# Performance work log

Hardware: AMD Instinct MI355X
Metric: run time of the kernel (lower is better)

The kernel has to match this reference:

```python
import jax, jax.numpy as jnp
import numpy as np

B, S, F, H, W = 16, 2048, 512, 512, 5
PAD = W // 2


def setup_inputs() -> dict:
    key = jax.random.key(0)
    k = jax.random.split(key, 6)
    scale = 0.02
    return {
        "embeds_output": jax.random.normal(k[0], (B, S, F), dtype=jnp.float32),
        "Wq": jax.random.normal(k[1], (F, H), dtype=jnp.float32) * scale,
        "Wk": jax.random.normal(k[2], (F, H), dtype=jnp.float32) * scale,
        "v_att": jax.random.normal(k[3], (H,), dtype=jnp.float32) * scale,
        "cnn_W": jax.random.normal(k[4], (W * F, H), dtype=jnp.float32) * scale,
        "cnn_b": jax.random.normal(k[5], (H,), dtype=jnp.float32) * scale,
    }


def reference(embeds_output, Wq, Wk, v_att, cnn_W, cnn_b):
    b, s, f = embeds_output.shape
    # getConvEmbeds: zero-pad and gather W shifted views -> [B, S, W, F]
    xp = jnp.pad(embeds_output, ((0, 0), (PAD, PAD), (0, 0)))
    windows = jnp.stack([xp[:, i:i + s, :] for i in range(W)], axis=2)  # [B,S,W,F]
    entity = windows[:, :, PAD, :]  # center token, [B,S,F]
    # Bahdanau additive attention over the window
    q = jnp.einsum('bsf,fh->bsh', entity, Wq)          # [B,S,H]
    kproj = jnp.einsum('bswf,fh->bswh', windows, Wk)   # [B,S,W,H]
    scores = jnp.einsum('bswh,h->bsw', jnp.tanh(kproj + q[:, :, None, :]), v_att)
    att = jax.nn.softmax(scores, axis=-1)              # [B,S,W]
    # weight contexts, flatten window dim (row-major W*F, matching torch reshape)
    att_context = (att[..., None] * windows).reshape(b, s, W * F)
    return att_context @ cnn_W + cnn_b                 # [B,S,H]
```

## Files before the change

### kernel.cpp

```cpp
#include <hip/hip_runtime.h>
#include <stdint.h>
#include <stddef.h>

typedef unsigned short u16;
typedef __attribute__((ext_vector_type(8))) short s16x8;
typedef __attribute__((ext_vector_type(8))) unsigned short u16x8;
typedef __attribute__((ext_vector_type(4))) unsigned short u16x4;
typedef __attribute__((ext_vector_type(4))) float f32x4;

typedef __attribute__((address_space(3))) void* as3_void_p;
typedef const __attribute__((address_space(1))) void* as1_cvoid_p;

#define GLD16(gp, lp) __builtin_amdgcn_global_load_lds((as1_cvoid_p)(gp), (as3_void_p)(lp), 16, 0, 0)

enum {
  NS = 2048, NF = 512, NH = 512, NW = 5,
  NROW = 32768,
  K2 = NW * NF
};

__device__ __forceinline__ u16 f2bf(float f) {
  unsigned u = __float_as_uint(f);
  u += 0x7FFFu + ((u >> 16) & 1u);
  return (u16)(u >> 16);
}
__device__ __forceinline__ float bf2f(u16 v) {
  return __uint_as_float(((unsigned)v) << 16);
}


__global__ __launch_bounds__(256) void cvtX(const float* __restrict__ X, u16* __restrict__ Xb) {
  int i = blockIdx.x * 256 + threadIdx.x;
  f32x4 v = ((const f32x4*)X)[i];
  u16x4 o;
  o.x = f2bf(v.x); o.y = f2bf(v.y); o.z = f2bf(v.z); o.w = f2bf(v.w);
  ((u16x4*)Xb)[i] = o;
}

__global__ __launch_bounds__(256) void cvtW(const float* __restrict__ Wq, const float* __restrict__ Wk,
                                            const float* __restrict__ cnnW,
                                            u16* __restrict__ Wt1, u16* __restrict__ Wt2) {
  int i = blockIdx.x * 256 + threadIdx.x;
  if (i < 1024 * 512) {
    int j = i >> 9, f = i & 511;
    float v = (j < 512) ? Wq[(size_t)f * 512 + j] : Wk[(size_t)f * 512 + (j - 512)];
    Wt1[i] = f2bf(v);
  } else {
    int t = i - 1024 * 512;
    int h = t / K2, k = t % K2;
    Wt2[t] = f2bf(cnnW[(size_t)k * 512 + h]);
  }
}


__global__ __launch_bounds__(512, 4) void gemm_qk(const u16* __restrict__ Xb,
                                                  const u16* __restrict__ Wt1,
                                                  u16* __restrict__ QKb) {
  __shared__ u16 As[2][128 * 64];
  __shared__ u16 Bs[2][128 * 64];
  const int tid  = threadIdx.x;
  const int lane = tid & 63, wid = tid >> 6;
  const int wr = wid >> 2, wc = wid & 3;
  const int fr = lane & 15, fq = lane >> 4;
  const int wgid = (blockIdx.x & 7) * 256 + (blockIdx.x >> 3);
  const int brow = (wgid >> 3) * 128;
  const int bcol = (wgid & 7) * 128;

  const int rsub = tid >> 3;
  const int cb   = (((tid & 7) ^ (rsub & 7)) << 4);
  const char* gA0 = (const char*)(Xb  + (size_t)(brow + rsub) * NF) + cb;
  const char* gA1 = (const char*)(Xb  + (size_t)(brow + 64 + rsub) * NF) + cb;
  const char* gB0 = (const char*)(Wt1 + (size_t)(bcol + rsub) * NF) + cb;
  const char* gB1 = (const char*)(Wt1 + (size_t)(bcol + 64 + rsub) * NF) + cb;

  f32x4 acc[4][2] = {};

  GLD16(gA0, (char*)As[0] + tid * 16);
  GLD16(gA1, (char*)As[0] + 8192 + tid * 16);
  GLD16(gB0, (char*)Bs[0] + tid * 16);
  GLD16(gB1, (char*)Bs[0] + 8192 + tid * 16);
  __syncthreads();

  int cur = 0;
  for (int kt = 0; kt < 8; ++kt) {
    if (kt + 1 < 8) {
      int o = (kt + 1) * 128;
      GLD16(gA0 + o, (char*)As[cur ^ 1] + tid * 16);
      GLD16(gA1 + o, (char*)As[cur ^ 1] + 8192 + tid * 16);
      GLD16(gB0 + o, (char*)Bs[cur ^ 1] + tid * 16);
      GLD16(gB1 + o, (char*)Bs[cur ^ 1] + 8192 + tid * 16);
    }
    const char* Ab = (const char*)As[cur];
    const char* Bb = (const char*)Bs[cur];
#pragma unroll
    for (int kk = 0; kk < 2; ++kk) {
      s16x8 af[4], bfr[2];
#pragma unroll
      for (int m = 0; m < 4; ++m) {
        int row = wr * 64 + m * 16 + fr;
        af[m] = *(const s16x8*)(Ab + row * 128 + ((kk * 64 + fq * 16) ^ ((row & 7) << 4)));
      }
#pragma unroll
      for (int n = 0; n < 2; ++n) {
        int row = wc * 32 + n * 16 + fr;
        bfr[n] = *(const s16x8*)(Bb + row * 128 + ((kk * 64 + fq * 16) ^ ((row & 7) << 4)));
      }
#pragma unroll
      for (int m = 0; m < 4; ++m)
#pragma unroll
        for (int n = 0; n < 2; ++n)
          acc[m][n] = __builtin_amdgcn_mfma_f32_16x16x32_bf16(af[m], bfr[n], acc[m][n], 0, 0, 0);
    }
    __syncthreads();
    cur ^= 1;
  }

#pragma unroll
  for (int m = 0; m < 4; ++m)
#pragma unroll
    for (int n = 0; n < 2; ++n)
#pragma unroll
      for (int r = 0; r < 4; ++r) {
        int row = brow + wr * 64 + m * 16 + fq * 4 + r;
        int col = bcol + wc * 32 + n * 16 + fr;
        QKb[(size_t)row * 1024 + col] = f2bf(acc[m][n][r]);
      }
}


__global__ __launch_bounds__(256) void scores_att(const u16* __restrict__ QKb,
                                                  const float* __restrict__ vatt,
                                                  float* __restrict__ att) {
  const int lane = threadIdx.x & 63;
  const int wid  = threadIdx.x >> 6;
  const int n = blockIdx.x * 4 + wid;
  const int s = n & (NS - 1);
  const int h0 = lane * 8;

  u16x8 qv = *(const u16x8*)(QKb + (size_t)n * 1024 + h0);
  f32x4 va0 = *(const f32x4*)(vatt + h0);
  f32x4 va1 = *(const f32x4*)(vatt + h0 + 4);
  float q[8], vv[8];
#pragma unroll
  for (int j = 0; j < 8; ++j) q[j] = bf2f(qv[j]);
  vv[0] = va0.x; vv[1] = va0.y; vv[2] = va0.z; vv[3] = va0.w;
  vv[4] = va1.x; vv[5] = va1.y; vv[6] = va1.z; vv[7] = va1.w;

  float sc[5];
#pragma unroll
  for (int w = 0; w < 5; ++w) {
    int sp = s + w - 2;
    u16x8 kv = {0, 0, 0, 0, 0, 0, 0, 0};
    if (sp >= 0 && sp < NS)
      kv = *(const u16x8*)(QKb + (size_t)(n + w - 2) * 1024 + 512 + h0);
    float acc = 0.f;
#pragma unroll
    for (int j = 0; j < 8; ++j) {
      float x = q[j] + bf2f(kv[j]);
      x = fminf(fmaxf(x, -15.f), 15.f);
      float e = __expf(2.f * x);
      acc += vv[j] * ((e - 1.f) / (e + 1.f));
    }
    sc[w] = acc;
  }
#pragma unroll
  for (int w = 0; w < 5; ++w)
#pragma unroll
    for (int o = 32; o > 0; o >>= 1)
      sc[w] += __shfl_xor(sc[w], o, 64);

  if (lane == 0) {
    float m = sc[0];
#pragma unroll
    for (int w = 1; w < 5; ++w) m = fmaxf(m, sc[w]);
    float e[5], sum = 0.f;
#pragma unroll
    for (int w = 0; w < 5; ++w) { e[w] = __expf(sc[w] - m); sum += e[w]; }
    float inv = 1.f / sum;
#pragma unroll
    for (int w = 0; w < 5; ++w) att[(size_t)n * 5 + w] = e[w] * inv;
  }
}


__global__ __launch_bounds__(512, 4) void gemm_out(const u16* __restrict__ Xb,
                                                   const u16* __restrict__ Wt2,
                                                   const float* __restrict__ att,
                                                   const float* __restrict__ cnnb,
                                                   float* __restrict__ out) {
  __shared__ u16 As[2][128 * 64];
  __shared__ u16 Bs[2][128 * 64];
  __shared__ float att_s[128 * 5];
  const int tid  = threadIdx.x;
  const int lane = tid & 63, wid = tid >> 6;
  const int wr = wid >> 2, wc = wid & 3;
  const int fr = lane & 15, fq = lane >> 4;
  const int wgid = (blockIdx.x & 7) * 128 + (blockIdx.x >> 3);
  const int brow = (wgid >> 2) * 128;
  const int bcol = (wgid & 3) * 128;

  if (tid < 128) {
    int s = (brow + tid) & (NS - 1);
#pragma unroll
    for (int w = 0; w < 5; ++w) {
      int sp = s + w - 2;
      att_s[tid * 5 + w] = (sp >= 0 && sp < NS) ? att[(size_t)(brow + tid) * 5 + w] : 0.f;
    }
  }

  const int rsub = tid >> 3;
  const int cb   = (((tid & 7) ^ (rsub & 7)) << 4);
  const char* gB0 = (const char*)(Wt2 + (size_t)(bcol + rsub) * K2) + cb;
  const char* gB1 = (const char*)(Wt2 + (size_t)(bcol + 64 + rsub) * K2) + cb;

  auto stage = [&](int buf, int it) {
    int wn = it >> 3, ktn = it & 7;
    int g0 = brow + rsub + wn - 2;
    int g1 = brow + 64 + rsub + wn - 2;
    g0 = g0 < 0 ? 0 : (g0 >= NROW ? NROW - 1 : g0);
    g1 = g1 < 0 ? 0 : (g1 >= NROW ? NROW - 1 : g1);
    int ko = ktn * 128;
    GLD16((const char*)(Xb + (size_t)g0 * NF) + cb + ko, (char*)As[buf] + tid * 16);
    GLD16((const char*)(Xb + (size_t)g1 * NF) + cb + ko, (char*)As[buf] + 8192 + tid * 16);
    GLD16(gB0 + wn * 1024 + ko, (char*)Bs[buf] + tid * 16);
    GLD16(gB1 + wn * 1024 + ko, (char*)Bs[buf] + 8192 + tid * 16);
  };

  f32x4 acc[4][2] = {};
  f32x4 accOut[4][2] = {};

  stage(0, 0);
  __syncthreads();

  int cur = 0;
  for (int it = 0; it < 40; ++it) {
    if (it + 1 < 40) stage(cur ^ 1, it + 1);
    const char* Ab = (const char*)As[cur];
    const char* Bb = (const char*)Bs[cur];
#pragma unroll
    for (int kk = 0; kk < 2; ++kk) {
      s16x8 af[4], bfr[2];
#pragma unroll
      for (int m = 0; m < 4; ++m) {
        int row = wr * 64 + m * 16 + fr;
        af[m] = *(const s16x8*)(Ab + row * 128 + ((kk * 64 + fq * 16) ^ ((row & 7) << 4)));
      }
#pragma unroll
      for (int n = 0; n < 2; ++n) {
        int row = wc * 32 + n * 16 + fr;
        bfr[n] = *(const s16x8*)(Bb + row * 128 + ((kk * 64 + fq * 16) ^ ((row & 7) << 4)));
      }
#pragma unroll
      for (int m = 0; m < 4; ++m)
#pragma unroll
        for (int n = 0; n < 2; ++n)
          acc[m][n] = __builtin_amdgcn_mfma_f32_16x16x32_bf16(af[m], bfr[n], acc[m][n], 0, 0, 0);
    }
    if ((it & 7) == 7) {
      int w = it >> 3;
#pragma unroll
      for (int m = 0; m < 4; ++m) {
        float a0 = att_s[(wr * 64 + m * 16 + fq * 4 + 0) * 5 + w];
        float a1 = att_s[(wr * 64 + m * 16 + fq * 4 + 1) * 5 + w];
        float a2 = att_s[(wr * 64 + m * 16 + fq * 4 + 2) * 5 + w];
        float a3 = att_s[(wr * 64 + m * 16 + fq * 4 + 3) * 5 + w];
#pragma unroll
        for (int n = 0; n < 2; ++n) {
          accOut[m][n][0] += a0 * acc[m][n][0];
          accOut[m][n][1] += a1 * acc[m][n][1];
          accOut[m][n][2] += a2 * acc[m][n][2];
          accOut[m][n][3] += a3 * acc[m][n][3];
          acc[m][n] = f32x4{0.f, 0.f, 0.f, 0.f};
        }
      }
    }
    __syncthreads();
    cur ^= 1;
  }

#pragma unroll
  for (int m = 0; m < 4; ++m)
#pragma unroll
    for (int n = 0; n < 2; ++n)
#pragma unroll
      for (int r = 0; r < 4; ++r) {
        int row = brow + wr * 64 + m * 16 + fq * 4 + r;
        int col = bcol + wc * 32 + n * 16 + fr;
        out[(size_t)row * NH + col] = accOut[m][n][r] + cnnb[col];
      }
}


extern "C" void kernel_launch(void* const* d_in, const int* in_sizes, int n_in,
                              void* d_out, int out_size, void* d_ws, size_t ws_size,
                              hipStream_t stream) {
  const float* X    = (const float*)d_in[0];
  const float* Wq   = (const float*)d_in[1];
  const float* Wk   = (const float*)d_in[2];
  const float* vatt = (const float*)d_in[3];
  const float* cnnW = (const float*)d_in[4];
  const float* cnnb = (const float*)d_in[5];
  float* out = (float*)d_out;

  char* ws = (char*)d_ws;
  u16*   Xb  = (u16*)ws;
  u16*   Wt1 = (u16*)(ws + 33554432);
  u16*   Wt2 = (u16*)(ws + 34603008);
  u16*   QKb = (u16*)(ws + 37224448);
  float* att = (float*)(ws + 104333312);

  cvtX<<<dim3(NROW * NF / 4 / 256), dim3(256), 0, stream>>>(X, Xb);
  cvtW<<<dim3((1024 * 512 + 512 * K2) / 256), dim3(256), 0, stream>>>(Wq, Wk, cnnW, Wt1, Wt2);
  gemm_qk<<<dim3(2048), dim3(512), 0, stream>>>(Xb, Wt1, QKb);
  scores_att<<<dim3(NROW / 4), dim3(256), 0, stream>>>(QKb, vatt, att);
  gemm_out<<<dim3(1024), dim3(512), 0, stream>>>(Xb, Wt2, att, cnnb, out);
}
```

Measured before the change: 215.2 us.

## Replace double-buffered BK=64 staging with single-buffered BK=128 tiles in both GEMMs

Both GEMM kernels drop the two-stage LDS double buffer with K-tiles of 64 and use a single buffer holding K-tiles of 128, loaded as four 32-row chunks per operand. This halves the number of K iterations and barriers per tile, while the LDS footprint stays the same. The cost is that global-to-LDS loads no longer overlap with MFMA work inside a block, so latency hiding now depends on other resident blocks. The output GEMM also restructures its loop into explicit window and K-tile nests.

```diff
diff --git a/kernel.cpp b/kernel.cpp
--- a/kernel.cpp
+++ b/kernel.cpp
@@ -56,8 +56,8 @@
 __global__ __launch_bounds__(512, 4) void gemm_qk(const u16* __restrict__ Xb,
                                                   const u16* __restrict__ Wt1,
                                                   u16* __restrict__ QKb) {
-  __shared__ u16 As[2][128 * 64];
-  __shared__ u16 Bs[2][128 * 64];
+  __shared__ u16 As[128 * 128];
+  __shared__ u16 Bs[128 * 128];
   const int tid  = threadIdx.x;
   const int lane = tid & 63, wid = tid >> 6;
   const int wr = wid >> 2, wc = wid & 3;
@@ -66,44 +66,38 @@
   const int brow = (wgid >> 3) * 128;
   const int bcol = (wgid & 7) * 128;
 
-  const int rsub = tid >> 3;
-  const int cb   = (((tid & 7) ^ (rsub & 7)) << 4);
-  const char* gA0 = (const char*)(Xb  + (size_t)(brow + rsub) * NF) + cb;
-  const char* gA1 = (const char*)(Xb  + (size_t)(brow + 64 + rsub) * NF) + cb;
-  const char* gB0 = (const char*)(Wt1 + (size_t)(bcol + rsub) * NF) + cb;
-  const char* gB1 = (const char*)(Wt1 + (size_t)(bcol + 64 + rsub) * NF) + cb;
+  const int rsub = tid >> 4;
+  const int scb  = ((tid & 15) << 4) ^ ((rsub & 7) << 4);
+  const char* gA[4];
+  const char* gB[4];
+#pragma unroll
+  for (int c = 0; c < 4; ++c) {
+    gA[c] = (const char*)(Xb  + (size_t)(brow + c * 32 + rsub) * NF) + scb;
+    gB[c] = (const char*)(Wt1 + (size_t)(bcol + c * 32 + rsub) * NF) + scb;
+  }
 
   f32x4 acc[4][2] = {};
 
-  GLD16(gA0, (char*)As[0] + tid * 16);
-  GLD16(gA1, (char*)As[0] + 8192 + tid * 16);
-  GLD16(gB0, (char*)Bs[0] + tid * 16);
-  GLD16(gB1, (char*)Bs[0] + 8192 + tid * 16);
-  __syncthreads();
-
-  int cur = 0;
-  for (int kt = 0; kt < 8; ++kt) {
-    if (kt + 1 < 8) {
-      int o = (kt + 1) * 128;
-      GLD16(gA0 + o, (char*)As[cur ^ 1] + tid * 16);
-      GLD16(gA1 + o, (char*)As[cur ^ 1] + 8192 + tid * 16);
-      GLD16(gB0 + o, (char*)Bs[cur ^ 1] + tid * 16);
-      GLD16(gB1 + o, (char*)Bs[cur ^ 1] + 8192 + tid * 16);
-    }
-    const char* Ab = (const char*)As[cur];
-    const char* Bb = (const char*)Bs[cur];
-#pragma unroll
-    for (int kk = 0; kk < 2; ++kk) {
+  for (int kt = 0; kt < 4; ++kt) {
+    const int ko = kt * 256;
+#pragma unroll
+    for (int c = 0; c < 4; ++c) {
+      GLD16(gA[c] + ko, (char*)As + c * 8192 + tid * 16);
+      GLD16(gB[c] + ko, (char*)Bs + c * 8192 + tid * 16);
+    }
+    __syncthreads();
+#pragma unroll
+    for (int kk = 0; kk < 4; ++kk) {
       s16x8 af[4], bfr[2];
 #pragma unroll
       for (int m = 0; m < 4; ++m) {
         int row = wr * 64 + m * 16 + fr;
-        af[m] = *(const s16x8*)(Ab + row * 128 + ((kk * 64 + fq * 16) ^ ((row & 7) << 4)));
+        af[m] = *(const s16x8*)((const char*)As + row * 256 + ((kk * 64 + fq * 16) ^ ((row & 7) << 4)));
       }
 #pragma unroll
       for (int n = 0; n < 2; ++n) {
         int row = wc * 32 + n * 16 + fr;
-        bfr[n] = *(const s16x8*)(Bb + row * 128 + ((kk * 64 + fq * 16) ^ ((row & 7) << 4)));
+        bfr[n] = *(const s16x8*)((const char*)Bs + row * 256 + ((kk * 64 + fq * 16) ^ ((row & 7) << 4)));
       }
 #pragma unroll
       for (int m = 0; m < 4; ++m)
@@ -112,7 +106,6 @@
           acc[m][n] = __builtin_amdgcn_mfma_f32_16x16x32_bf16(af[m], bfr[n], acc[m][n], 0, 0, 0);
     }
     __syncthreads();
-    cur ^= 1;
   }
 
 #pragma unroll
@@ -188,8 +181,8 @@
                                                    const float* __restrict__ att,
                                                    const float* __restrict__ cnnb,
                                                    float* __restrict__ out) {
-  __shared__ u16 As[2][128 * 64];
-  __shared__ u16 Bs[2][128 * 64];
+  __shared__ u16 As[128 * 128];
+  __shared__ u16 Bs[128 * 128];
   __shared__ float att_s[128 * 5];
   const int tid  = threadIdx.x;
   const int lane = tid & 63, wid = tid >> 6;
@@ -208,74 +201,70 @@
     }
   }
 
-  const int rsub = tid >> 3;
-  const int cb   = (((tid & 7) ^ (rsub & 7)) << 4);
-  const char* gB0 = (const char*)(Wt2 + (size_t)(bcol + rsub) * K2) + cb;
-  const char* gB1 = (const char*)(Wt2 + (size_t)(bcol + 64 + rsub) * K2) + cb;
-
-  auto stage = [&](int buf, int it) {
-    int wn = it >> 3, ktn = it & 7;
-    int g0 = brow + rsub + wn - 2;
-    int g1 = brow + 64 + rsub + wn - 2;
-    g0 = g0 < 0 ? 0 : (g0 >= NROW ? NROW - 1 : g0);
-    g1 = g1 < 0 ? 0 : (g1 >= NROW ? NROW - 1 : g1);
-    int ko = ktn * 128;
-    GLD16((const char*)(Xb + (size_t)g0 * NF) + cb + ko, (char*)As[buf] + tid * 16);
-    GLD16((const char*)(Xb + (size_t)g1 * NF) + cb + ko, (char*)As[buf] + 8192 + tid * 16);
-    GLD16(gB0 + wn * 1024 + ko, (char*)Bs[buf] + tid * 16);
-    GLD16(gB1 + wn * 1024 + ko, (char*)Bs[buf] + 8192 + tid * 16);
-  };
+  const int rsub = tid >> 4;
+  const int scb  = ((tid & 15) << 4) ^ ((rsub & 7) << 4);
+  const char* gB[4];
+#pragma unroll
+  for (int c = 0; c < 4; ++c)
+    gB[c] = (const char*)(Wt2 + (size_t)(bcol + c * 32 + rsub) * K2) + scb;
 
   f32x4 acc[4][2] = {};
   f32x4 accOut[4][2] = {};
 
-  stage(0, 0);
-  __syncthreads();
-
-  int cur = 0;
-  for (int it = 0; it < 40; ++it) {
-    if (it + 1 < 40) stage(cur ^ 1, it + 1);
-    const char* Ab = (const char*)As[cur];
-    const char* Bb = (const char*)Bs[cur];
-#pragma unroll
-    for (int kk = 0; kk < 2; ++kk) {
-      s16x8 af[4], bfr[2];
-#pragma unroll
-      for (int m = 0; m < 4; ++m) {
-        int row = wr * 64 + m * 16 + fr;
-        af[m] = *(const s16x8*)(Ab + row * 128 + ((kk * 64 + fq * 16) ^ ((row & 7) << 4)));
-      }
+  for (int w = 0; w < 5; ++w) {
+    const char* gA[4];
+#pragma unroll
+    for (int c = 0; c < 4; ++c) {
+      int g = brow + c * 32 + rsub + w - 2;
+      g = g < 0 ? 0 : (g >= NROW ? NROW - 1 : g);
+      gA[c] = (const char*)(Xb + (size_t)g * NF) + scb;
+    }
+    const int wo = w * 1024;
+
+    for (int kt = 0; kt < 4; ++kt) {
+      const int ko = kt * 256;
+#pragma unroll
+      for (int c = 0; c < 4; ++c) {
+        GLD16(gA[c] + ko,      (char*)As + c * 8192 + tid * 16);
+        GLD16(gB[c] + wo + ko, (char*)Bs + c * 8192 + tid * 16);
+      }
+      __syncthreads();
+#pragma unroll
+      for (int kk = 0; kk < 4; ++kk) {
+        s16x8 af[4], bfr[2];
+#pragma unroll
+        for (int m = 0; m < 4; ++m) {
+          int row = wr * 64 + m * 16 + fr;
+          af[m] = *(const s16x8*)((const char*)As + row * 256 + ((kk * 64 + fq * 16) ^ ((row & 7) << 4)));
+        }
+#pragma unroll
+        for (int n = 0; n < 2; ++n) {
+          int row = wc * 32 + n * 16 + fr;
+          bfr[n] = *(const s16x8*)((const char*)Bs + row * 256 + ((kk * 64 + fq * 16) ^ ((row & 7) << 4)));
+        }
+#pragma unroll
+        for (int m = 0; m < 4; ++m)
+#pragma unroll
+          for (int n = 0; n < 2; ++n)
+            acc[m][n] = __builtin_amdgcn_mfma_f32_16x16x32_bf16(af[m], bfr[n], acc[m][n], 0, 0, 0);
+      }
+      __syncthreads();
+    }
+#pragma unroll
+    for (int m = 0; m < 4; ++m) {
+      float a0 = att_s[(wr * 64 + m * 16 + fq * 4 + 0) * 5 + w];
+      float a1 = att_s[(wr * 64 + m * 16 + fq * 4 + 1) * 5 + w];
+      float a2 = att_s[(wr * 64 + m * 16 + fq * 4 + 2) * 5 + w];
+      float a3 = att_s[(wr * 64 + m * 16 + fq * 4 + 3) * 5 + w];
 #pragma unroll
       for (int n = 0; n < 2; ++n) {
-        int row = wc * 32 + n * 16 + fr;
-        bfr[n] = *(const s16x8*)(Bb + row * 128 + ((kk * 64 + fq * 16) ^ ((row & 7) << 4)));
-      }
-#pragma unroll
-      for (int m = 0; m < 4; ++m)
-#pragma unroll
-        for (int n = 0; n < 2; ++n)
-          acc[m][n] = __builtin_amdgcn_mfma_f32_16x16x32_bf16(af[m], bfr[n], acc[m][n], 0, 0, 0);
-    }
-    if ((it & 7) == 7) {
-      int w = it >> 3;
-#pragma unroll
-      for (int m = 0; m < 4; ++m) {
-        float a0 = att_s[(wr * 64 + m * 16 + fq * 4 + 0) * 5 + w];
-        float a1 = att_s[(wr * 64 + m * 16 + fq * 4 + 1) * 5 + w];
-        float a2 = att_s[(wr * 64 + m * 16 + fq * 4 + 2) * 5 + w];
-        float a3 = att_s[(wr * 64 + m * 16 + fq * 4 + 3) * 5 + w];
-#pragma unroll
-        for (int n = 0; n < 2; ++n) {
-          accOut[m][n][0] += a0 * acc[m][n][0];
-          accOut[m][n][1] += a1 * acc[m][n][1];
-          accOut[m][n][2] += a2 * acc[m][n][2];
-          accOut[m][n][3] += a3 * acc[m][n][3];
-          acc[m][n] = f32x4{0.f, 0.f, 0.f, 0.f};
-        }
-      }
-    }
-    __syncthreads();
-    cur ^= 1;
+        accOut[m][n][0] += a0 * acc[m][n][0];
+        accOut[m][n][1] += a1 * acc[m][n][1];
+        accOut[m][n][2] += a2 * acc[m][n][2];
+        accOut[m][n][3] += a3 * acc[m][n][3];
+        acc[m][n] = f32x4{0.f, 0.f, 0.f, 0.f};
+      }
+    }
   }
 
 #pragma unroll
```

Result: faster. 210.7 us (-2.1%).
